# Optimization experiments

Hardware: AMD Instinct MI355X
Metric: run time of the kernel (lower is better)

## Reference

```python
import jax, jax.numpy as jnp
import numpy as np


def _resize_hw(x, h, w):
    # PyTorch F.interpolate(mode='bilinear', align_corners=False) == half-pixel
    # bilinear without antialiasing.
    return jax.image.resize(x, x.shape[:-2] + (h, w), method='bilinear', antialias=False)


def _make_char_mask(attn, fore_mask, alpha):
    # attn: [b,26,w_attn] float; fore_mask: [b,1,H,W] int32
    W = fore_mask.shape[-1]
    attn_i = _resize_hw(attn[:, None], 26, W)[:, 0]          # [b,26,W]
    attn_b = (attn_i > alpha).astype(jnp.int32)              # threshold
    single = attn_b[:, :, None, :] * fore_mask               # [b,26,H,W]
    return jnp.concatenate([1 - fore_mask, single], axis=1)  # [b,27,H,W]


def _loss(char_feature, mask, length):
    # char_feature: [b,27,H,W] logits; mask: [b,27,H,W] int; length: [b]
    c = char_feature.shape[1]
    target = jnp.argmax(mask, axis=1)                         # [b,H,W] (first-max, same as torch)
    logp = jax.nn.log_softmax(char_feature, axis=1)
    ce = -jnp.mean(jnp.take_along_axis(logp, target[:, None], axis=1))
    prob = jnp.exp(logp)
    m = mask.astype(prob.dtype)
    smooth = 1.0
    inter = jnp.sum(prob * m, axis=(2, 3))                    # [b,27]
    s1 = jnp.sum(prob, axis=(2, 3))
    s2 = jnp.sum(m, axis=(2, 3))
    score = (2.0 * inter + smooth) / (s1 + s2 + smooth)       # [b,27]
    lens = length - 1                                          # chars per sample
    ch = jnp.arange(c)
    valid = (ch[None, :] >= 1) & (ch[None, :] <= lens[:, None])  # channels 1..len
    per_sample = jnp.sum((1.0 - score) * valid, axis=1) / lens.astype(prob.dtype)
    dice = jnp.mean(per_sample)
    return ce + dice


def setup_inputs() -> dict:
    key = jax.random.key(0)
    k1, k2, k3, k4, k5 = jax.random.split(key, 5)
    b = 512
    return {
        'char_feature_mid': jax.random.normal(k1, (b, 27, 32, 128), dtype=jnp.float32),
        'char_feature_low': jax.random.normal(k2, (b, 27, 16, 64), dtype=jnp.float32),
        'seq1_attention_map': jax.random.uniform(k3, (b, 26, 32), dtype=jnp.float32),
        'fore_mask': jax.random.uniform(k4, (b, 1, 32, 128), dtype=jnp.float32),
        'length': jax.random.randint(k5, (b,), 2, 27),
        'alpha': jnp.float32(0.3),
    }


def reference(char_feature_mid, char_feature_low, seq1_attention_map, fore_mask, length, alpha):
    h_mid, w_mid = char_feature_mid.shape[-2:]
    h_low, w_low = char_feature_low.shape[-2:]
    # clear_noise: zero attention rows at index >= length-1
    keep = jnp.arange(seq1_attention_map.shape[1])[None, :] < (length - 1)[:, None]
    attn = seq1_attention_map * keep[..., None].astype(seq1_attention_map.dtype)
    # low-resolution branch
    fm_low = (_resize_hw(fore_mask, h_low, w_low) >= 0.4).astype(jnp.int32)
    mask_low = _make_char_mask(attn, fm_low, alpha)
    loss_low = _loss(char_feature_low, mask_low, length)
    # middle-resolution branch
    fm_mid = (_resize_hw(fore_mask, h_mid, w_mid) >= 0.4).astype(jnp.int32)
    mask_mid = _make_char_mask(attn, fm_mid, alpha)
    loss_middle = _loss(char_feature_mid, mask_mid, length)
    return ((loss_low, loss_middle), mask_low)
```

## Files before the change

kernel.cpp:

```cpp
#include <hip/hip_runtime.h>
#include <stdint.h>


#define DPP_ADD(v, ctrl)                                                      \
  v += __int_as_float(__builtin_amdgcn_update_dpp(                            \
      0, __float_as_int(v), (ctrl), 0xf, 0xf, true))

static __device__ __forceinline__ float dpp_reduce_add(float v) {
  DPP_ADD(v, 0xB1);
  DPP_ADD(v, 0x4E);
  DPP_ADD(v, 0x141);
  DPP_ADD(v, 0x140);
  DPP_ADD(v, 0x142);
  DPP_ADD(v, 0x143);
  return v;
}

static __device__ __forceinline__ float wave_reduce_add(float v) {
  v += __shfl_xor(v, 1, 64);
  v += __shfl_xor(v, 2, 64);
  v += __shfl_xor(v, 4, 64);
  v += __shfl_xor(v, 8, 64);
  v += __shfl_xor(v, 16, 64);
  v += __shfl_xor(v, 32, 64);
  return v;
}

static __device__ __forceinline__ uint32_t attn_bits(const float* sattn, float src,
                                                     int lens, float alpha) {
  const int k0 = (int)floorf(src);
  uint32_t bits = 0u;
  if (k0 < 0 || k0 >= 31) {
    const int kk = (k0 < 0) ? 0 : 31;
    for (int c = 0; c < 26; ++c) {
      float v = (c < lens) ? sattn[c * 32 + kk] : 0.0f;
      if (v > alpha) bits |= (1u << c);
    }
  } else {
    const float frac = src - (float)k0;
    const float w1 = frac, w0 = 1.0f - frac;
    for (int c = 0; c < 26; ++c) {
      float v = __fadd_rn(__fmul_rn(w0, sattn[c * 32 + k0]),
                          __fmul_rn(w1, sattn[c * 32 + k0 + 1]));
      v = (c < lens) ? v : 0.0f;
      if (v > alpha) bits |= (1u << c);
    }
  }
  return bits;
}

__global__ __launch_bounds__(192) void prep_kernel(
    const float* __restrict__ attn,
    const float* __restrict__ fore,
    const int* __restrict__ length,
    const float* __restrict__ alpha_p,
    uint32_t* __restrict__ bits_mid,
    uint32_t* __restrict__ bits_low,
    float* __restrict__ acc_mid,
    float* __restrict__ acc_low,
    float* __restrict__ ce) {
  __shared__ float sattn[26 * 32];
  __shared__ int scnt_mid[128];
  __shared__ int scnt_low[64];
  __shared__ uint32_t sbits_mid[128];
  __shared__ uint32_t sbits_low[64];
  const int b = blockIdx.x;
  const int t = threadIdx.x;
  for (int i = t; i < 832; i += 192) sattn[i] = attn[b * 832 + i];
  if (t < 54) { acc_mid[b * 81 + t] = 0.0f; acc_low[b * 81 + t] = 0.0f; }
  if (b == 0 && t >= 96 && t < 98) ce[t - 96] = 0.0f;

  const float* fb = fore + (size_t)b * 4096;
  if (t < 128) {
    int cnt = 0;
    for (int y = 0; y < 32; ++y) cnt += (fb[y * 128 + t] >= 0.4f) ? 1 : 0;
    scnt_mid[t] = cnt;
  } else {
    const int x = t - 128;
    int cnt = 0;
    for (int y = 0; y < 16; ++y) {
      const float2* fr = (const float2*)(fb + (size_t)(2 * y) * 128 + 2 * x);
      const float2 f0 = fr[0];
      const float2 f1 = fr[64];
      const float t0 = __fadd_rn(0.5f * f0.x, 0.5f * f1.x);
      const float t1 = __fadd_rn(0.5f * f0.y, 0.5f * f1.y);
      const float fmv = __fadd_rn(0.5f * t0, 0.5f * t1);
      cnt += (fmv >= 0.4f) ? 1 : 0;
    }
    scnt_low[x] = cnt;
  }
  __syncthreads();

  const float alpha = alpha_p[0];
  const int lens = length[b] - 1;
  if (t < 128) {
    const float src = 0.25f * (float)t - 0.375f;
    const uint32_t bits = attn_bits(sattn, src, lens, alpha);
    bits_mid[b * 128 + t] = bits;
    sbits_mid[t] = bits;
  } else {
    const int x = t - 128;
    const float src = 0.5f * (float)x - 0.25f;
    const uint32_t bits = attn_bits(sattn, src, lens, alpha);
    bits_low[b * 64 + x] = bits;
    sbits_low[x] = bits;
  }
  __syncthreads();

  if (t < 27) {
    const int c = t;
    int s2;
    if (c == 0) {
      int tot = 0;
      for (int x = 0; x < 128; ++x) tot += scnt_mid[x];
      s2 = 4096 - tot;
    } else {
      s2 = 0;
      for (int x = 0; x < 128; ++x)
        s2 += (int)((sbits_mid[x] >> (c - 1)) & 1u) * scnt_mid[x];
    }
    acc_mid[b * 81 + 54 + c] = (float)s2;
  } else if (t >= 64 && t < 91) {
    const int c = t - 64;
    int s2;
    if (c == 0) {
      int tot = 0;
      for (int x = 0; x < 64; ++x) tot += scnt_low[x];
      s2 = 1024 - tot;
    } else {
      s2 = 0;
      for (int x = 0; x < 64; ++x)
        s2 += (int)((sbits_low[x] >> (c - 1)) & 1u) * scnt_low[x];
    }
    acc_low[b * 81 + 54 + c] = (float)s2;
  }
}

__global__ __launch_bounds__(256) void main_kernel(
    const float* __restrict__ cf_mid,
    const float* __restrict__ cf_low,
    const float* __restrict__ fore,
    float* __restrict__ out,
    const uint32_t* __restrict__ bits_mid,
    const uint32_t* __restrict__ bits_low,
    float* __restrict__ acc_mid,
    float* __restrict__ acc_low,
    float* __restrict__ ce) {
  const int t = threadIdx.x;
  const int bid = blockIdx.x;
  const bool low = (bid >= 4096);
  int b, p0, W, HW;
  const float* cf;
  const uint32_t* bitsp;
  float* acc;
  if (low) {
    const int idx = bid - 4096;
    b = idx >> 1; p0 = (idx & 1) << 9; W = 64; HW = 1024;
    cf = cf_low; bitsp = bits_low + (size_t)b * 64; acc = acc_low;
  } else {
    b = bid >> 3; p0 = (bid & 7) << 9; W = 128; HW = 4096;
    cf = cf_mid; bitsp = bits_mid + (size_t)b * 128; acc = acc_mid;
  }
  const float* cfb = cf + (size_t)b * 27 * HW;
  const float* fb = fore + (size_t)b * 4096;
  float* mout = out + 2 + (size_t)b * 27 * 1024;

  float inter[27], s1[27];
#pragma unroll
  for (int c = 0; c < 27; ++c) { inter[c] = 0.0f; s1[c] = 0.0f; }
  float cesum = 0.0f;

  for (int k = 0; k < 2; ++k) {
    const int p = p0 + t + (k << 8);
    const int x = p & (W - 1);

    int fmw;
    if (low) {
      const int y = p >> 6;
      const float2* fr = (const float2*)(fb + (size_t)(2 * y) * 128 + 2 * x);
      const float2 f0 = fr[0];
      const float2 f1 = fr[64];
      const float t0 = __fadd_rn(0.5f * f0.x, 0.5f * f1.x);
      const float t1 = __fadd_rn(0.5f * f0.y, 0.5f * f1.y);
      const float fmv = __fadd_rn(0.5f * t0, 0.5f * t1);
      fmw = (fmv >= 0.4f) ? 1 : 0;
    } else {
      fmw = (fb[p] >= 0.4f) ? 1 : 0;
    }

    const uint32_t bits = bitsp[x];
    const int target = fmw ? (int)__ffs(bits) : 0;

    float l[27];
    float m = -1e30f, lt = 0.0f;
#pragma unroll
    for (int c = 0; c < 27; ++c) {
      const float v = cfb[(size_t)c * HW + p];
      l[c] = v;
      m = fmaxf(m, v);
      lt = (c == target) ? v : lt;
    }
    float s = 0.0f;
#pragma unroll
    for (int c = 0; c < 27; ++c) {
      const float e = __expf(l[c] - m);
      l[c] = e;
      s += e;
    }
    const float inv = 1.0f / s;
    cesum += (m + __logf(s) - lt);

#pragma unroll
    for (int c = 0; c < 27; ++c) {
      const float prob = l[c] * inv;
      s1[c] += prob;
      float mf;
      if (c == 0) mf = (float)(1 - fmw);
      else mf = (float)(((bits >> (c - 1)) & 1u) & (uint32_t)fmw);
      inter[c] += prob * mf;
      if (low) mout[(size_t)c * 1024 + p] = mf;
    }
  }

  __shared__ float red[4][55];
  const int wave = t >> 6, lane = t & 63;
#pragma unroll
  for (int c = 0; c < 27; ++c) {
    inter[c] = dpp_reduce_add(inter[c]);
    s1[c] = dpp_reduce_add(s1[c]);
  }
  cesum = dpp_reduce_add(cesum);
  if (lane == 63) {
#pragma unroll
    for (int c = 0; c < 27; ++c) {
      red[wave][c] = inter[c];
      red[wave][27 + c] = s1[c];
    }
    red[wave][54] = cesum;
  }
  __syncthreads();
  if (t < 55) {
    const float v = red[0][t] + red[1][t] + red[2][t] + red[3][t];
    if (t == 54) atomicAdd(&ce[low ? 0 : 1], v);
    else atomicAdd(&acc[(size_t)b * 81 + t], v);
  }
}

__global__ __launch_bounds__(256) void final_kernel(
    const float* __restrict__ acc_mid,
    const float* __restrict__ acc_low,
    const float* __restrict__ ce,
    const int* __restrict__ length,
    float* __restrict__ out) {
  const int B = blockIdx.x;
  const float* acc = (B == 0) ? acc_low : acc_mid;
  const float hw = (B == 0) ? 1024.0f : 4096.0f;
  const int t = threadIdx.x;
  float dsum = 0.0f;
  for (int b = t; b < 512; b += 256) {
    const int lens = length[b] - 1;
    const float* a = acc + (size_t)b * 81;
    float d = 0.0f;
    for (int c = 1; c < 27; ++c) {
      const float I = a[c], S1 = a[27 + c], S2 = a[54 + c];
      const float score = (2.0f * I + 1.0f) / (S1 + S2 + 1.0f);
      if (c <= lens) d += (1.0f - score);
    }
    dsum += d / (float)lens;
  }
  __shared__ float red[4];
  const int wave = t >> 6, lane = t & 63;
  dsum = wave_reduce_add(dsum);
  if (lane == 0) red[wave] = dsum;
  __syncthreads();
  if (t == 0) {
    const float dice = red[0] + red[1] + red[2] + red[3];
    out[B] = dice * (1.0f / 512.0f) + ce[B] * (1.0f / (512.0f * hw));
  }
}

extern "C" void kernel_launch(void* const* d_in, const int* in_sizes, int n_in,
                              void* d_out, int out_size, void* d_ws, size_t ws_size,
                              hipStream_t stream) {
  const float* cf_mid = (const float*)d_in[0];
  const float* cf_low = (const float*)d_in[1];
  const float* attn   = (const float*)d_in[2];
  const float* fore   = (const float*)d_in[3];
  const int*   length = (const int*)d_in[4];
  const float* alpha  = (const float*)d_in[5];
  float* out = (float*)d_out;

  uint32_t* bits_mid = (uint32_t*)d_ws;
  uint32_t* bits_low = bits_mid + 512 * 128;
  float* acc_mid = (float*)(bits_low + 512 * 64);
  float* acc_low = acc_mid + 512 * 81;
  float* ce = acc_low + 512 * 81;

  hipLaunchKernelGGL(prep_kernel, dim3(512), dim3(192), 0, stream,
                     attn, fore, length, alpha, bits_mid, bits_low,
                     acc_mid, acc_low, ce);
  hipLaunchKernelGGL(main_kernel, dim3(5120), dim3(256), 0, stream,
                     cf_mid, cf_low, fore, out, bits_mid, bits_low,
                     acc_mid, acc_low, ce);
  hipLaunchKernelGGL(final_kernel, dim3(2), dim3(256), 0, stream,
                     acc_mid, acc_low, ce, length, out);
}
```

Baseline: 392.2 us.

## Stage logits tile into LDS via async global_load_lds before softmax

Each block now copies its 27x512 logit tile from global memory straight into shared memory with 16-byte global_load_lds, then waits once and runs the softmax, CE and dice sums from LDS. The foreground mask, attention bits and target are computed while those loads are in flight. The aim is to put all of the block's memory traffic in flight at once instead of issuing 27 strided 4-byte loads per pixel. In exchange the block uses about 55KB of LDS, which limits how many blocks fit on a CU.

```diff
diff --git a/kernel.cpp b/kernel.cpp
--- a/kernel.cpp
+++ b/kernel.cpp
@@ -146,7 +146,11 @@
     float* __restrict__ acc_mid,
     float* __restrict__ acc_low,
     float* __restrict__ ce) {
+  __shared__ float sl[27 * 512];
+  __shared__ float red[4][55];
   const int t = threadIdx.x;
+  const int lane = t & 63;
+  const int wave = t >> 6;
   const int bid = blockIdx.x;
   const bool low = (bid >= 4096);
   int b, p0, W, HW;
@@ -165,15 +169,28 @@
   const float* fb = fore + (size_t)b * 4096;
   float* mout = out + 2 + (size_t)b * 27 * 1024;
 
-  float inter[27], s1[27];
-#pragma unroll
-  for (int c = 0; c < 27; ++c) { inter[c] = 0.0f; s1[c] = 0.0f; }
-  float cesum = 0.0f;
-
+  {
+    const uint8_t* cfb_b = (const uint8_t*)cfb + (size_t)p0 * 4;
+    uint8_t* sl_b = (uint8_t*)sl;
+    const size_t cstride = (size_t)HW * 4;
+    for (int j = wave; j < 54; j += 4) {
+      const int chunk = (j << 6) + lane;
+      const uint8_t* g =
+          cfb_b + (size_t)(chunk >> 7) * cstride + ((chunk & 127) << 4);
+      __builtin_amdgcn_global_load_lds(
+          (const __attribute__((address_space(1))) void*)g,
+          (__attribute__((address_space(3))) void*)(sl_b + ((size_t)j << 10)),
+          16, 0, 0);
+    }
+  }
+
+  int fmw2[2];
+  uint32_t bits2[2];
+  int tgt2[2];
+#pragma unroll
   for (int k = 0; k < 2; ++k) {
     const int p = p0 + t + (k << 8);
     const int x = p & (W - 1);
-
     int fmw;
     if (low) {
       const int y = p >> 6;
@@ -187,15 +204,32 @@
     } else {
       fmw = (fb[p] >= 0.4f) ? 1 : 0;
     }
-
     const uint32_t bits = bitsp[x];
-    const int target = fmw ? (int)__ffs(bits) : 0;
+    fmw2[k] = fmw;
+    bits2[k] = bits;
+    tgt2[k] = fmw ? (int)__ffs(bits) : 0;
+  }
+
+  asm volatile("s_waitcnt vmcnt(0)");
+  __syncthreads();
+
+  float inter[27], s1[27];
+#pragma unroll
+  for (int c = 0; c < 27; ++c) { inter[c] = 0.0f; s1[c] = 0.0f; }
+  float cesum = 0.0f;
+
+  for (int k = 0; k < 2; ++k) {
+    const int px = t + (k << 8);
+    const int p = p0 + px;
+    const int fmw = fmw2[k];
+    const uint32_t bits = bits2[k];
+    const int target = tgt2[k];
 
     float l[27];
     float m = -1e30f, lt = 0.0f;
 #pragma unroll
     for (int c = 0; c < 27; ++c) {
-      const float v = cfb[(size_t)c * HW + p];
+      const float v = sl[c * 512 + px];
       l[c] = v;
       m = fmaxf(m, v);
       lt = (c == target) ? v : lt;
@@ -222,8 +256,6 @@
     }
   }
 
-  __shared__ float red[4][55];
-  const int wave = t >> 6, lane = t & 63;
 #pragma unroll
   for (int c = 0; c < 27; ++c) {
     inter[c] = dpp_reduce_add(inter[c]);
```

Result: no change. 394.7 us (+0.6%).

## Process four pixels per thread with float4 loads and three-pass softmax re-reads

Applied to the files above, without the earlier changes.

Each thread now handles four contiguous pixels and loads logits and stores mask outputs as float4, which halves the grid and widens memory transactions. Instead of keeping 27 logits per pixel in registers, the kernel makes three passes over global memory (max, exp-sum, then prob and accumulation) and recomputes exp in the last pass. This is meant to lower register pressure and improve load vectorization, at the cost of reading the inputs three times (relying on cache hits) and doing extra exp work.

```diff
diff --git a/kernel.cpp b/kernel.cpp
--- a/kernel.cpp
+++ b/kernel.cpp
@@ -146,34 +146,36 @@
     float* __restrict__ acc_mid,
     float* __restrict__ acc_low,
     float* __restrict__ ce) {
+  __shared__ float red[4][55];
   const int t = threadIdx.x;
+  const int lane = t & 63;
+  const int wave = t >> 6;
   const int bid = blockIdx.x;
-  const bool low = (bid >= 4096);
+  const bool low = (bid >= 2048);
   int b, p0, W, HW;
   const float* cf;
   const uint32_t* bitsp;
   float* acc;
   if (low) {
-    const int idx = bid - 4096;
-    b = idx >> 1; p0 = (idx & 1) << 9; W = 64; HW = 1024;
+    b = bid - 2048; p0 = 0; W = 64; HW = 1024;
     cf = cf_low; bitsp = bits_low + (size_t)b * 64; acc = acc_low;
   } else {
-    b = bid >> 3; p0 = (bid & 7) << 9; W = 128; HW = 4096;
+    b = bid >> 2; p0 = (bid & 3) << 10; W = 128; HW = 4096;
     cf = cf_mid; bitsp = bits_mid + (size_t)b * 128; acc = acc_mid;
   }
   const float* cfb = cf + (size_t)b * 27 * HW;
   const float* fb = fore + (size_t)b * 4096;
   float* mout = out + 2 + (size_t)b * 27 * 1024;
 
-  float inter[27], s1[27];
-#pragma unroll
-  for (int c = 0; c < 27; ++c) { inter[c] = 0.0f; s1[c] = 0.0f; }
-  float cesum = 0.0f;
-
-  for (int k = 0; k < 2; ++k) {
-    const int p = p0 + t + (k << 8);
+  const int pbase = p0 + (t << 2);
+  const float* cp = cfb + pbase;
+
+  int fmw4[4], tgt4[4];
+  uint32_t bits4[4];
+#pragma unroll
+  for (int j = 0; j < 4; ++j) {
+    const int p = pbase + j;
     const int x = p & (W - 1);
-
     int fmw;
     if (low) {
       const int y = p >> 6;
@@ -187,43 +189,68 @@
     } else {
       fmw = (fb[p] >= 0.4f) ? 1 : 0;
     }
-
     const uint32_t bits = bitsp[x];
-    const int target = fmw ? (int)__ffs(bits) : 0;
-
-    float l[27];
-    float m = -1e30f, lt = 0.0f;
-#pragma unroll
-    for (int c = 0; c < 27; ++c) {
-      const float v = cfb[(size_t)c * HW + p];
-      l[c] = v;
-      m = fmaxf(m, v);
-      lt = (c == target) ? v : lt;
-    }
-    float s = 0.0f;
-#pragma unroll
-    for (int c = 0; c < 27; ++c) {
-      const float e = __expf(l[c] - m);
-      l[c] = e;
-      s += e;
-    }
-    const float inv = 1.0f / s;
-    cesum += (m + __logf(s) - lt);
-
-#pragma unroll
-    for (int c = 0; c < 27; ++c) {
-      const float prob = l[c] * inv;
+    fmw4[j] = fmw;
+    bits4[j] = bits;
+    tgt4[j] = fmw ? (int)__ffs(bits) : 0;
+  }
+
+  float m4[4] = {-1e30f, -1e30f, -1e30f, -1e30f};
+  float lt4[4] = {0.0f, 0.0f, 0.0f, 0.0f};
+#pragma unroll
+  for (int c = 0; c < 27; ++c) {
+    const float4 v = *(const float4*)(cp + (size_t)c * HW);
+    const float vv[4] = {v.x, v.y, v.z, v.w};
+#pragma unroll
+    for (int j = 0; j < 4; ++j) {
+      m4[j] = fmaxf(m4[j], vv[j]);
+      lt4[j] = (c == tgt4[j]) ? vv[j] : lt4[j];
+    }
+  }
+  asm volatile("" ::: "memory");
+
+  float s4[4] = {0.0f, 0.0f, 0.0f, 0.0f};
+#pragma unroll
+  for (int c = 0; c < 27; ++c) {
+    const float4 v = *(const float4*)(cp + (size_t)c * HW);
+    const float vv[4] = {v.x, v.y, v.z, v.w};
+#pragma unroll
+    for (int j = 0; j < 4; ++j) s4[j] += __expf(vv[j] - m4[j]);
+  }
+  float inv4[4];
+  float cesum = 0.0f;
+#pragma unroll
+  for (int j = 0; j < 4; ++j) {
+    inv4[j] = 1.0f / s4[j];
+    cesum += (m4[j] + __logf(s4[j]) - lt4[j]);
+  }
+  asm volatile("" ::: "memory");
+
+  float inter[27], s1[27];
+#pragma unroll
+  for (int c = 0; c < 27; ++c) { inter[c] = 0.0f; s1[c] = 0.0f; }
+#pragma unroll
+  for (int c = 0; c < 27; ++c) {
+    const float4 v = *(const float4*)(cp + (size_t)c * HW);
+    const float vv[4] = {v.x, v.y, v.z, v.w};
+    float mf4[4];
+#pragma unroll
+    for (int j = 0; j < 4; ++j) {
+      const float prob = __expf(vv[j] - m4[j]) * inv4[j];
       s1[c] += prob;
       float mf;
-      if (c == 0) mf = (float)(1 - fmw);
-      else mf = (float)(((bits >> (c - 1)) & 1u) & (uint32_t)fmw);
+      if (c == 0) mf = (float)(1 - fmw4[j]);
+      else mf = (float)(((bits4[j] >> (c - 1)) & 1u) & (uint32_t)fmw4[j]);
       inter[c] += prob * mf;
-      if (low) mout[(size_t)c * 1024 + p] = mf;
-    }
-  }
-
-  __shared__ float red[4][55];
-  const int wave = t >> 6, lane = t & 63;
+      mf4[j] = mf;
+    }
+    if (low) {
+      float4 st;
+      st.x = mf4[0]; st.y = mf4[1]; st.z = mf4[2]; st.w = mf4[3];
+      *(float4*)(mout + (size_t)c * 1024 + pbase) = st;
+    }
+  }
+
 #pragma unroll
   for (int c = 0; c < 27; ++c) {
     inter[c] = dpp_reduce_add(inter[c]);
@@ -299,7 +326,7 @@
   hipLaunchKernelGGL(prep_kernel, dim3(512), dim3(192), 0, stream,
                      attn, fore, length, alpha, bits_mid, bits_low,
                      acc_mid, acc_low, ce);
-  hipLaunchKernelGGL(main_kernel, dim3(5120), dim3(256), 0, stream,
+  hipLaunchKernelGGL(main_kernel, dim3(2560), dim3(256), 0, stream,
                      cf_mid, cf_low, fore, out, bits_mid, bits_low,
                      acc_mid, acc_low, ce);
   hipLaunchKernelGGL(final_kernel, dim3(2), dim3(256), 0, stream,
```

Result: slower. 421.1 us (+7.4%).
